# Kernel tuning notes

Measured on AMD Instinct MI355X. Metric: run time of the kernel, lower is better.

## Reference

```python
import jax, jax.numpy as jnp
import numpy as np

NEG_SLOPE = 0.2


def gat_conv(x, src, dst, W, a_src, a_dst, b, num_nodes):
    # x: [N, Fin], W: [Fin, Fout], a_src/a_dst: [Fout], b: [Fout]
    h = x @ W                                   # [N, Fout]
    alpha_s = h @ a_src                         # [N]
    alpha_d = h @ a_dst                         # [N]
    e = alpha_s[src] + alpha_d[dst]             # [E]
    e = jnp.where(e > 0, e, NEG_SLOPE * e)      # LeakyReLU(0.2)
    # segment softmax over edges grouped by destination node
    m = jax.ops.segment_max(e, dst, num_segments=num_nodes)   # [N]
    e = jnp.exp(e - m[dst])
    s = jax.ops.segment_sum(e, dst, num_segments=num_nodes)   # [N]
    alpha = e / s[dst]                          # [E] (every node has a self-loop)
    out = jax.ops.segment_sum(h[src] * alpha[:, None], dst, num_segments=num_nodes)
    return out + b


def setup_inputs() -> dict:
    key = jax.random.key(0)
    ks = jax.random.split(key, 10)
    N, E = 50000, 640000
    Fin, Fh, Fout = 128, 128, 64
    x = jax.random.normal(ks[0], (N, Fin), dtype=jnp.float32)
    edge_index = jax.random.randint(ks[1], (2, E), 0, N, dtype=jnp.int64)
    g = 1.0 / np.sqrt(Fin)
    W1 = jax.random.normal(ks[2], (Fin, Fh), dtype=jnp.float32) * g
    a1_src = jax.random.normal(ks[3], (Fh,), dtype=jnp.float32) * 0.1
    a1_dst = jax.random.normal(ks[4], (Fh,), dtype=jnp.float32) * 0.1
    b1 = jnp.zeros((Fh,), dtype=jnp.float32)
    g2 = 1.0 / np.sqrt(Fh)
    W2 = jax.random.normal(ks[5], (Fh, Fout), dtype=jnp.float32) * g2
    a2_src = jax.random.normal(ks[6], (Fout,), dtype=jnp.float32) * 0.1
    a2_dst = jax.random.normal(ks[7], (Fout,), dtype=jnp.float32) * 0.1
    b2 = jnp.zeros((Fout,), dtype=jnp.float32)
    return {"x": x, "edge_index": edge_index, "W1": W1, "a1_src": a1_src,
            "a1_dst": a1_dst, "b1": b1, "W2": W2, "a2_src": a2_src,
            "a2_dst": a2_dst, "b2": b2}


def reference(x, edge_index, W1, a1_src, a1_dst, b1, W2, a2_src, a2_dst, b2):
    N = x.shape[0]
    loops = jnp.arange(N, dtype=edge_index.dtype)
    src = jnp.concatenate([edge_index[0], loops])  # add self-loops (PyG default)
    dst = jnp.concatenate([edge_index[1], loops])
    h = gat_conv(x, src, dst, W1, a1_src, a1_dst, b1, N)
    h = jax.nn.relu(h)
    # F.dropout(0.1) skipped: deterministic (eval-mode) reference
    out = gat_conv(h, src, dst, W2, a2_src, a2_dst, b2, N)
    return out
```

## Files before the change

### kernel.cpp

```cpp
#include <hip/hip_runtime.h>

#define LEAK 0.2f

static __device__ __forceinline__ float leaky(float e) { return e > 0.f ? e : LEAK * e; }

static __device__ __forceinline__ unsigned f2bf(float f) {
    union { float f; unsigned u; } v; v.f = f;
    return (v.u + 0x7FFFu + ((v.u >> 16) & 1u)) >> 16;
}
static __device__ __forceinline__ float bflo(unsigned u) {
    union { unsigned x; float f; } v; v.x = u << 16; return v.f;
}
static __device__ __forceinline__ float bfhi(unsigned u) {
    union { unsigned x; float f; } v; v.x = u & 0xFFFF0000u; return v.f;
}

using bf16x8 = __attribute__((ext_vector_type(8))) short;
using f32x4 = __attribute__((ext_vector_type(4))) float;

__global__ __launch_bounds__(256) void k_prep(int* __restrict__ counts, int n,
                                              const int* __restrict__ ei, int nwords_check,
                                              int* __restrict__ flag,
                                              const float* __restrict__ W1,
                                              unsigned short* __restrict__ Wt1,
                                              const float* __restrict__ W2,
                                              unsigned short* __restrict__ Wt2, int NB) {
    int bid = blockIdx.x;
    int t = threadIdx.x;
    if (bid == 0) {
        if (t < 64) {
            int bad = 0;
            for (int i = 1 + 2 * t; i < nwords_check; i += 128) bad |= (ei[i] != 0);
            unsigned long long anybad = __ballot(bad != 0);
            if (t == 0) *flag = (anybad == 0ULL) ? 1 : 0;
        }
        return;
    }
    if (bid <= NB) {
        int i = (bid - 1) * 256 + t;
        if (i < n) counts[i] = 0;
        return;
    }
    if (bid <= NB + 4) {
        int q = bid - (NB + 1);
        int c = t & 127, ksub = t >> 7;
        int k0 = q * 32 + ksub * 16;
        union { unsigned short s[16]; uint4 v[2]; } u;
#pragma unroll
        for (int j = 0; j < 16; ++j) u.s[j] = (unsigned short)f2bf(W1[(size_t)(k0 + j) * 128 + c]);
        uint4* dst = (uint4*)(Wt1 + (size_t)c * 128 + k0);
        dst[0] = u.v[0];
        dst[1] = u.v[1];
        return;
    }
    {
        int q = bid - (NB + 5);
        int c = t & 63, ksub = t >> 6;
        int k0 = q * 64 + ksub * 16;
        union { unsigned short s[16]; uint4 v[2]; } u;
#pragma unroll
        for (int j = 0; j < 16; ++j) u.s[j] = (unsigned short)f2bf(W2[(size_t)(k0 + j) * 64 + c]);
        uint4* dst = (uint4*)(Wt2 + (size_t)c * 128 + k0);
        dst[0] = u.v[0];
        dst[1] = u.v[1];
        return;
    }
}

__global__ __launch_bounds__(256) void k_rank(const int* __restrict__ ei,
                                              const int* __restrict__ flag,
                                              int* __restrict__ counts,
                                              int* __restrict__ rank_,
                                              int* __restrict__ srcv,
                                              int* __restrict__ dstv, int E) {
    int base = (blockIdx.x * 256 + threadIdx.x) * 4;
    if (base >= E) return;
    int is64 = *flag;
    if (base + 3 < E) {
        int s0, s1, s2, s3, d0, d1, d2, d3;
        if (is64) {
            const uint4* ps = (const uint4*)(ei + 2 * (size_t)base);
            uint4 a = ps[0], b = ps[1];
            const uint4* pd = (const uint4*)(ei + 2 * ((size_t)E + base));
            uint4 c = pd[0], e4 = pd[1];
            s0 = a.x; s1 = a.z; s2 = b.x; s3 = b.z;
            d0 = c.x; d1 = c.z; d2 = e4.x; d3 = e4.z;
        } else {
            int4 a = *(const int4*)(ei + base);
            int4 b = *(const int4*)(ei + (size_t)E + base);
            s0 = a.x; s1 = a.y; s2 = a.z; s3 = a.w;
            d0 = b.x; d1 = b.y; d2 = b.z; d3 = b.w;
        }
        int r0 = atomicAdd(&counts[d0], 1);
        int r1 = atomicAdd(&counts[d1], 1);
        int r2 = atomicAdd(&counts[d2], 1);
        int r3 = atomicAdd(&counts[d3], 1);
        *(int4*)(rank_ + base) = make_int4(r0, r1, r2, r3);
        *(int4*)(srcv + base) = make_int4(s0, s1, s2, s3);
        *(int4*)(dstv + base) = make_int4(d0, d1, d2, d3);
    } else {
        for (int j = 0; j < 4 && base + j < E; ++j) {
            int e = base + j;
            int ss = is64 ? ei[2 * (size_t)e] : ei[e];
            int dd = is64 ? ei[2 * ((size_t)E + e)] : ei[(size_t)E + e];
            int r = atomicAdd(&counts[dd], 1);
            rank_[e] = r;
            srcv[e] = ss;
            dstv[e] = dd;
        }
    }
}

__global__ void k_scan1(const int* __restrict__ counts, int* __restrict__ incl,
                        int* __restrict__ bsums, int n) {
    __shared__ int s[256];
    int t = threadIdx.x;
    int g = blockIdx.x * 256 + t;
    int v = (g < n) ? counts[g] : 0;
    s[t] = v;
    __syncthreads();
    for (int off = 1; off < 256; off <<= 1) {
        int add = (t >= off) ? s[t - off] : 0;
        __syncthreads();
        s[t] += add;
        __syncthreads();
    }
    if (g < n) incl[g] = s[t];
    if (t == 255) bsums[blockIdx.x] = s[255];
}

__global__ void k_scan2(int* __restrict__ bsums, int nb) {
    __shared__ int s[256];
    int t = threadIdx.x;
    int v = (t < nb) ? bsums[t] : 0;
    s[t] = v;
    __syncthreads();
    for (int off = 1; off < 256; off <<= 1) {
        int add = (t >= off) ? s[t - off] : 0;
        __syncthreads();
        s[t] += add;
        __syncthreads();
    }
    int excl = (t == 0) ? 0 : s[t - 1];
    if (t < nb) bsums[t] = excl;
}

__global__ void k_scan3(const int* __restrict__ incl, const int* __restrict__ bsums,
                        int* __restrict__ rowptr, int n) {
    int g = blockIdx.x * 256 + threadIdx.x;
    if (g < n) rowptr[g + 1] = incl[g] + bsums[blockIdx.x];
    if (g == 0) rowptr[0] = 0;
}

__global__ __launch_bounds__(256) void k_place(const int* __restrict__ rank_,
                                               const int* __restrict__ srcv,
                                               const int* __restrict__ dstv,
                                               const int* __restrict__ rowptr,
                                               int* __restrict__ colv, int E) {
    int base = (blockIdx.x * 256 + threadIdx.x) * 4;
    if (base >= E) return;
    if (base + 3 < E) {
        int4 r = *(const int4*)(rank_ + base);
        int4 s = *(const int4*)(srcv + base);
        int4 d = *(const int4*)(dstv + base);
        int p0 = rowptr[d.x] + r.x;
        int p1 = rowptr[d.y] + r.y;
        int p2 = rowptr[d.z] + r.z;
        int p3 = rowptr[d.w] + r.w;
        colv[p0] = s.x;
        colv[p1] = s.y;
        colv[p2] = s.z;
        colv[p3] = s.w;
    } else {
        for (int j = 0; j < 4 && base + j < E; ++j) {
            int e = base + j;
            colv[rowptr[dstv[e]] + rank_[e]] = srcv[e];
        }
    }
}

template <int F, bool AF32>
__global__ __launch_bounds__(256) void k_gemm_mfma(const void* __restrict__ Xv,
                                                   const unsigned short* __restrict__ Wt,
                                                   const float* __restrict__ asrc,
                                                   const float* __restrict__ adst,
                                                   unsigned short* __restrict__ Hb,
                                                   float* __restrict__ out_s,
                                                   float* __restrict__ out_d, int n) {
    constexpr int K = 128;
    constexpr int KP = K + 8;
    constexpr int NT = F / 16;
    __shared__ unsigned short wsT[F * KP];
    int t = threadIdx.x;
    int w = t >> 6, lane = t & 63;
    int lrow = lane & 15, kg = lane >> 4;
    long long row0 = (long long)blockIdx.x * 64;

#pragma unroll
    for (int i = t; i < F * (K / 8); i += 256) {
        int c = i / (K / 8), j8 = i % (K / 8);
        uint4 v = ((const uint4*)(Wt + (size_t)c * K))[j8];
        *(uint4*)&wsT[c * KP + 8 * j8] = v;
    }
    __syncthreads();

    long long grow = row0 + w * 16 + lrow;
    bool rowok = grow < n;

    f32x4 acc[NT];
#pragma unroll
    for (int i = 0; i < NT; ++i) acc[i] = (f32x4){0.f, 0.f, 0.f, 0.f};

#pragma unroll
    for (int ks = 0; ks < K / 32; ++ks) {
        bf16x8 af;
        if constexpr (AF32) {
            const float* Xp = (const float*)Xv + grow * K + ks * 32 + kg * 8;
            float4 x0 = make_float4(0.f, 0.f, 0.f, 0.f), x1 = x0;
            if (rowok) {
                x0 = ((const float4*)Xp)[0];
                x1 = ((const float4*)Xp)[1];
            }
            af = (bf16x8){(short)f2bf(x0.x), (short)f2bf(x0.y), (short)f2bf(x0.z), (short)f2bf(x0.w),
                          (short)f2bf(x1.x), (short)f2bf(x1.y), (short)f2bf(x1.z), (short)f2bf(x1.w)};
        } else {
            uint4 u = make_uint4(0, 0, 0, 0);
            if (rowok) {
                const unsigned short* Xp = (const unsigned short*)Xv + grow * K + ks * 32 + kg * 8;
                u = *(const uint4*)Xp;
            }
            af = *(bf16x8*)&u;
        }
#pragma unroll
        for (int nt = 0; nt < NT; ++nt) {
            const unsigned short* bp = &wsT[(nt * 16 + lrow) * KP + ks * 32 + kg * 8];
            uint4 ub = *(const uint4*)bp;
            bf16x8 bf = *(bf16x8*)&ub;
            acc[nt] = __builtin_amdgcn_mfma_f32_16x16x32_bf16(af, bf, acc[nt], 0, 0, 0);
        }
    }

    {
        float ps[4] = {0.f, 0.f, 0.f, 0.f}, pd[4] = {0.f, 0.f, 0.f, 0.f};
#pragma unroll
        for (int nt = 0; nt < NT; ++nt) {
            float asv = asrc[nt * 16 + lrow];
            float adv = adst[nt * 16 + lrow];
#pragma unroll
            for (int i = 0; i < 4; ++i) {
                ps[i] = fmaf(acc[nt][i], asv, ps[i]);
                pd[i] = fmaf(acc[nt][i], adv, pd[i]);
            }
        }
#pragma unroll
        for (int off = 1; off < 16; off <<= 1) {
#pragma unroll
            for (int i = 0; i < 4; ++i) {
                ps[i] += __shfl_xor(ps[i], off);
                pd[i] += __shfl_xor(pd[i], off);
            }
        }
        if (lrow == 0) {
#pragma unroll
            for (int i = 0; i < 4; ++i) {
                long long r = row0 + w * 16 + kg * 4 + i;
                if (r < n) {
                    out_s[r] = ps[i];
                    out_d[r] = pd[i];
                }
            }
        }
    }

    int r0 = w * 16 + kg * 4;
#pragma unroll
    for (int nt = 0; nt < NT; ++nt) {
        int c = nt * 16 + lrow;
#pragma unroll
        for (int i = 0; i < 4; ++i) {
            long long r = row0 + r0 + i;
            if (r < n) Hb[r * F + c] = (unsigned short)f2bf(acc[nt][i]);
        }
    }
}

template <int F, bool RELU, bool OB>
__global__ __launch_bounds__(256) void k_agg(const int* __restrict__ rowptr,
                                             const int* __restrict__ colv,
                                             const float* __restrict__ as_,
                                             const float* __restrict__ ad_,
                                             const unsigned* __restrict__ Hu,
                                             const float* __restrict__ bias,
                                             void* __restrict__ OUT, int n) {
    constexpr int FG8 = F / 8;
    constexpr int GRP = 64 / FG8;
    int node = blockIdx.x * 4 + (threadIdx.x >> 6);
    int lane = threadIdx.x & 63;
    if (node >= n) return;
    int rs = rowptr[node], re = rowptr[node + 1];
    int deg = re - rs;
    float adi = ad_[node];
    float e_self = leaky(as_[node] + adi);

    int scol = node;
    float e_l = -3.0e38f;
    if (lane < deg) {
        scol = colv[rs + lane];
        e_l = leaky(as_[scol] + adi);
    }
    float m = fmaxf(e_l, e_self);
    for (int base = 64; base < deg; base += 64) {
        if (base + lane < deg) m = fmaxf(m, leaky(as_[colv[rs + base + lane]] + adi));
    }
#pragma unroll
    for (int off = 32; off; off >>= 1) m = fmaxf(m, __shfl_xor(m, off));

    float p_l = (lane < deg) ? __expf(e_l - m) : 0.f;
    float ssum = p_l;
    for (int base = 64; base < deg; base += 64) {
        if (base + lane < deg) ssum += __expf(leaky(as_[colv[rs + base + lane]] + adi) - m);
    }
#pragma unroll
    for (int off = 32; off; off >>= 1) ssum += __shfl_xor(ssum, off);
    float pself = __expf(e_self - m);
    ssum += pself;
    float inv = 1.f / ssum;
    float w_l = p_l * inv;
    float wself = pself * inv;

    int grp = lane / FG8;
    int fg = lane % FG8;
    const uint4* __restrict__ H16 = (const uint4*)Hu;
    float a0, a1, a2, a3, a4, a5, a6, a7;
    {
        uint4 hv = H16[(size_t)node * FG8 + fg];
        float ws0 = (grp == 0) ? wself : 0.f;
        a0 = ws0 * bflo(hv.x); a1 = ws0 * bfhi(hv.x);
        a2 = ws0 * bflo(hv.y); a3 = ws0 * bfhi(hv.y);
        a4 = ws0 * bflo(hv.z); a5 = ws0 * bfhi(hv.z);
        a6 = ws0 * bflo(hv.w); a7 = ws0 * bfhi(hv.w);
    }

    int cnt = deg < 64 ? deg : 64;
    constexpr int STEP = 4 * GRP;
    int cntr = (cnt + STEP - 1) / STEP * STEP;
#pragma unroll 1
    for (int i = 0; i < cntr; i += STEP) {
        int i0 = i + grp, i1 = i + GRP + grp, i2 = i + 2 * GRP + grp, i3 = i + 3 * GRP + grp;
        int s0 = __shfl(scol, i0), s1 = __shfl(scol, i1);
        int s2 = __shfl(scol, i2), s3 = __shfl(scol, i3);
        float w0 = __shfl(w_l, i0), w1 = __shfl(w_l, i1);
        float w2 = __shfl(w_l, i2), w3 = __shfl(w_l, i3);
        uint4 g0 = H16[(size_t)s0 * FG8 + fg];
        uint4 g1 = H16[(size_t)s1 * FG8 + fg];
        uint4 g2 = H16[(size_t)s2 * FG8 + fg];
        uint4 g3 = H16[(size_t)s3 * FG8 + fg];
        a0 = fmaf(w0, bflo(g0.x), a0); a1 = fmaf(w0, bfhi(g0.x), a1);
        a2 = fmaf(w0, bflo(g0.y), a2); a3 = fmaf(w0, bfhi(g0.y), a3);
        a4 = fmaf(w0, bflo(g0.z), a4); a5 = fmaf(w0, bfhi(g0.z), a5);
        a6 = fmaf(w0, bflo(g0.w), a6); a7 = fmaf(w0, bfhi(g0.w), a7);
        a0 = fmaf(w1, bflo(g1.x), a0); a1 = fmaf(w1, bfhi(g1.x), a1);
        a2 = fmaf(w1, bflo(g1.y), a2); a3 = fmaf(w1, bfhi(g1.y), a3);
        a4 = fmaf(w1, bflo(g1.z), a4); a5 = fmaf(w1, bfhi(g1.z), a5);
        a6 = fmaf(w1, bflo(g1.w), a6); a7 = fmaf(w1, bfhi(g1.w), a7);
        a0 = fmaf(w2, bflo(g2.x), a0); a1 = fmaf(w2, bfhi(g2.x), a1);
        a2 = fmaf(w2, bflo(g2.y), a2); a3 = fmaf(w2, bfhi(g2.y), a3);
        a4 = fmaf(w2, bflo(g2.z), a4); a5 = fmaf(w2, bfhi(g2.z), a5);
        a6 = fmaf(w2, bflo(g2.w), a6); a7 = fmaf(w2, bfhi(g2.w), a7);
        a0 = fmaf(w3, bflo(g3.x), a0); a1 = fmaf(w3, bfhi(g3.x), a1);
        a2 = fmaf(w3, bflo(g3.y), a2); a3 = fmaf(w3, bfhi(g3.y), a3);
        a4 = fmaf(w3, bflo(g3.z), a4); a5 = fmaf(w3, bfhi(g3.z), a5);
        a6 = fmaf(w3, bflo(g3.w), a6); a7 = fmaf(w3, bfhi(g3.w), a7);
    }
    for (int j = rs + 64; j < re; ++j) {
        int s = colv[j];
        float w = __expf(leaky(as_[s] + adi) - m) * inv;
        float we = (grp == 0) ? w : 0.f;
        uint4 g = H16[(size_t)s * FG8 + fg];
        a0 = fmaf(we, bflo(g.x), a0); a1 = fmaf(we, bfhi(g.x), a1);
        a2 = fmaf(we, bflo(g.y), a2); a3 = fmaf(we, bfhi(g.y), a3);
        a4 = fmaf(we, bflo(g.z), a4); a5 = fmaf(we, bfhi(g.z), a5);
        a6 = fmaf(we, bflo(g.w), a6); a7 = fmaf(we, bfhi(g.w), a7);
    }
#pragma unroll
    for (int off = FG8; off < 64; off <<= 1) {
        a0 += __shfl_xor(a0, off); a1 += __shfl_xor(a1, off);
        a2 += __shfl_xor(a2, off); a3 += __shfl_xor(a3, off);
        a4 += __shfl_xor(a4, off); a5 += __shfl_xor(a5, off);
        a6 += __shfl_xor(a6, off); a7 += __shfl_xor(a7, off);
    }
    if (grp == 0) {
        const float4* b4 = (const float4*)bias;
        float4 bv0 = b4[fg * 2], bv1 = b4[fg * 2 + 1];
        a0 += bv0.x; a1 += bv0.y; a2 += bv0.z; a3 += bv0.w;
        a4 += bv1.x; a5 += bv1.y; a6 += bv1.z; a7 += bv1.w;
        if (RELU) {
            a0 = fmaxf(a0, 0.f); a1 = fmaxf(a1, 0.f);
            a2 = fmaxf(a2, 0.f); a3 = fmaxf(a3, 0.f);
            a4 = fmaxf(a4, 0.f); a5 = fmaxf(a5, 0.f);
            a6 = fmaxf(a6, 0.f); a7 = fmaxf(a7, 0.f);
        }
        if (OB) {
            uint4 p;
            p.x = f2bf(a0) | (f2bf(a1) << 16);
            p.y = f2bf(a2) | (f2bf(a3) << 16);
            p.z = f2bf(a4) | (f2bf(a5) << 16);
            p.w = f2bf(a6) | (f2bf(a7) << 16);
            ((uint4*)OUT)[(size_t)node * FG8 + fg] = p;
        } else {
            float4* o4 = (float4*)((float*)OUT + (size_t)node * F + fg * 8);
            o4[0] = make_float4(a0, a1, a2, a3);
            o4[1] = make_float4(a4, a5, a6, a7);
        }
    }
}

extern "C" void kernel_launch(void* const* d_in, const int* in_sizes, int n_in,
                              void* d_out, int out_size, void* d_ws, size_t ws_size,
                              hipStream_t stream) {
    const float* x   = (const float*)d_in[0];
    const int*   ei  = (const int*)d_in[1];
    const float* W1  = (const float*)d_in[2];
    const float* a1s = (const float*)d_in[3];
    const float* a1d = (const float*)d_in[4];
    const float* b1  = (const float*)d_in[5];
    const float* W2  = (const float*)d_in[6];
    const float* a2s = (const float*)d_in[7];
    const float* a2d = (const float*)d_in[8];
    const float* b2  = (const float*)d_in[9];
    float* out = (float*)d_out;

    int N = in_sizes[0] / 128;
    int E = in_sizes[1] / 2;

    size_t off = 0;
    auto alloc = [&](size_t bytes) -> void* {
        off = (off + 255) & ~(size_t)255;
        void* p = (char*)d_ws + off;
        off += bytes;
        return p;
    };
    unsigned short* h = (unsigned short*)alloc((size_t)N * 128 * 2);
    unsigned short* out1b = (unsigned short*)alloc((size_t)N * 128 * 2);
    unsigned short* Wt1 = (unsigned short*)alloc(128 * 128 * 2);
    unsigned short* Wt2 = (unsigned short*)alloc(64 * 128 * 2);
    float* as_    = (float*)alloc((size_t)N * 4);
    float* ad_    = (float*)alloc((size_t)N * 4);
    int* counts   = (int*)alloc((size_t)N * 4);
    int* rowptr   = (int*)alloc((size_t)(N + 1) * 4);
    int* incl     = (int*)alloc((size_t)N * 4);
    int* bsums    = (int*)alloc(1024);
    int* colv     = (int*)alloc((size_t)E * 4);
    int* rank_    = (int*)alloc((size_t)E * 4);
    int* srcv     = (int*)alloc((size_t)E * 4);
    int* dstv     = (int*)alloc((size_t)E * 4);
    int* flag     = (int*)alloc(256);

    int NB = (N + 255) / 256;
    int blocksN4 = (N + 3) / 4;
    int rowTiles = (N + 63) / 64;
    int blocksE4 = (E + 1023) / 1024;

    int nchk = 2 * E < 512 ? 2 * E : 512;
    k_prep<<<NB + 7, 256, 0, stream>>>(counts, N, ei, nchk, flag, W1, Wt1, W2, Wt2, NB);
    k_rank<<<blocksE4, 256, 0, stream>>>(ei, flag, counts, rank_, srcv, dstv, E);
    k_scan1<<<NB, 256, 0, stream>>>(counts, incl, bsums, N);
    k_scan2<<<1, 256, 0, stream>>>(bsums, NB);
    k_scan3<<<NB, 256, 0, stream>>>(incl, bsums, rowptr, N);
    k_place<<<blocksE4, 256, 0, stream>>>(rank_, srcv, dstv, rowptr, colv, E);

    k_gemm_mfma<128, true><<<rowTiles, 256, 0, stream>>>(x, Wt1, a1s, a1d, h, as_, ad_, N);
    k_agg<128, true, true><<<blocksN4, 256, 0, stream>>>(rowptr, colv, as_, ad_,
                                                         (const unsigned*)h, b1, out1b, N);

    k_gemm_mfma<64, false><<<rowTiles, 256, 0, stream>>>(out1b, Wt2, a2s, a2d, h, as_, ad_, N);
    k_agg<64, false, false><<<blocksN4, 256, 0, stream>>>(rowptr, colv, as_, ad_,
                                                          (const unsigned*)h, b2, out, N);
}
```

Measured before the change: 139.7 us.

## Fuse CSR construction kernels into one cooperative kernel with grid syncs

Replaces the separate prep, rank, three-pass scan and place kernels with a single cooperative kernel. It uses grid-wide syncs between phases and runs a fixed grid of 256 blocks looping over the edges. Rank and destination are packed into one 32-bit word (rank in the high 16 bits, destination in the low 16), which removes the dstv and incl buffers and their memory traffic. The aim is to cut launch overhead and inter-kernel gaps. The trade-offs are grid.sync costs, less parallelism to hide atomic latency, and an implicit limit of N below 65536 and at most 256 scan chunks.

Result: slower. 250.1 us (+79.0%).

```diff
diff --git a/kernel.cpp b/kernel.cpp
--- a/kernel.cpp
+++ b/kernel.cpp
@@ -1,4 +1,7 @@
 #include <hip/hip_runtime.h>
+#include <hip/hip_cooperative_groups.h>
+
+namespace cg = cooperative_groups;
 
 #define LEAK 0.2f
 
@@ -18,163 +21,144 @@
 using bf16x8 = __attribute__((ext_vector_type(8))) short;
 using f32x4 = __attribute__((ext_vector_type(4))) float;
 
-__global__ __launch_bounds__(256) void k_prep(int* __restrict__ counts, int n,
-                                              const int* __restrict__ ei, int nwords_check,
-                                              int* __restrict__ flag,
-                                              const float* __restrict__ W1,
-                                              unsigned short* __restrict__ Wt1,
-                                              const float* __restrict__ W2,
-                                              unsigned short* __restrict__ Wt2, int NB) {
-    int bid = blockIdx.x;
-    int t = threadIdx.x;
+__global__ __launch_bounds__(256) void k_csr(const int* __restrict__ ei, int E, int N, int nchk,
+                                             int* __restrict__ flag, int* __restrict__ counts,
+                                             int* __restrict__ bsums, int* __restrict__ rowptr,
+                                             int* __restrict__ rankd, int* __restrict__ srcv,
+                                             int* __restrict__ colv,
+                                             const float* __restrict__ W1,
+                                             unsigned short* __restrict__ Wt1,
+                                             const float* __restrict__ W2,
+                                             unsigned short* __restrict__ Wt2) {
+    cg::grid_group grid = cg::this_grid();
+    __shared__ int s[256];
+    int t = threadIdx.x, bid = blockIdx.x;
+    int G = gridDim.x;
+    int gid = bid * 256 + t, GT = G * 256;
+
+    for (int i = gid; i < N; i += GT) counts[i] = 0;
     if (bid == 0) {
         if (t < 64) {
             int bad = 0;
-            for (int i = 1 + 2 * t; i < nwords_check; i += 128) bad |= (ei[i] != 0);
-            unsigned long long anybad = __ballot(bad != 0);
-            if (t == 0) *flag = (anybad == 0ULL) ? 1 : 0;
-        }
-        return;
-    }
-    if (bid <= NB) {
-        int i = (bid - 1) * 256 + t;
-        if (i < n) counts[i] = 0;
-        return;
-    }
-    if (bid <= NB + 4) {
-        int q = bid - (NB + 1);
+            for (int i = 1 + 2 * t; i < nchk; i += 128) bad |= (ei[i] != 0);
+            unsigned long long ab = __ballot(bad != 0);
+            if (t == 0) *flag = (ab == 0ULL) ? 1 : 0;
+        }
+    } else if (bid <= 4) {
+        int q = bid - 1;
         int c = t & 127, ksub = t >> 7;
         int k0 = q * 32 + ksub * 16;
-        union { unsigned short s[16]; uint4 v[2]; } u;
-#pragma unroll
-        for (int j = 0; j < 16; ++j) u.s[j] = (unsigned short)f2bf(W1[(size_t)(k0 + j) * 128 + c]);
+        union { unsigned short us[16]; uint4 v[2]; } u;
+#pragma unroll
+        for (int j = 0; j < 16; ++j) u.us[j] = (unsigned short)f2bf(W1[(size_t)(k0 + j) * 128 + c]);
         uint4* dst = (uint4*)(Wt1 + (size_t)c * 128 + k0);
         dst[0] = u.v[0];
         dst[1] = u.v[1];
-        return;
-    }
-    {
-        int q = bid - (NB + 5);
+    } else if (bid <= 6) {
+        int q = bid - 5;
         int c = t & 63, ksub = t >> 6;
         int k0 = q * 64 + ksub * 16;
-        union { unsigned short s[16]; uint4 v[2]; } u;
-#pragma unroll
-        for (int j = 0; j < 16; ++j) u.s[j] = (unsigned short)f2bf(W2[(size_t)(k0 + j) * 64 + c]);
+        union { unsigned short us[16]; uint4 v[2]; } u;
+#pragma unroll
+        for (int j = 0; j < 16; ++j) u.us[j] = (unsigned short)f2bf(W2[(size_t)(k0 + j) * 64 + c]);
         uint4* dst = (uint4*)(Wt2 + (size_t)c * 128 + k0);
         dst[0] = u.v[0];
         dst[1] = u.v[1];
-        return;
-    }
-}
-
-__global__ __launch_bounds__(256) void k_rank(const int* __restrict__ ei,
-                                              const int* __restrict__ flag,
-                                              int* __restrict__ counts,
-                                              int* __restrict__ rank_,
-                                              int* __restrict__ srcv,
-                                              int* __restrict__ dstv, int E) {
-    int base = (blockIdx.x * 256 + threadIdx.x) * 4;
-    if (base >= E) return;
-    int is64 = *flag;
-    if (base + 3 < E) {
-        int s0, s1, s2, s3, d0, d1, d2, d3;
-        if (is64) {
-            const uint4* ps = (const uint4*)(ei + 2 * (size_t)base);
-            uint4 a = ps[0], b = ps[1];
-            const uint4* pd = (const uint4*)(ei + 2 * ((size_t)E + base));
-            uint4 c = pd[0], e4 = pd[1];
-            s0 = a.x; s1 = a.z; s2 = b.x; s3 = b.z;
-            d0 = c.x; d1 = c.z; d2 = e4.x; d3 = e4.z;
+    }
+    grid.sync();
+
+    int is64 = *(volatile int*)flag;
+    for (long long base = (long long)gid * 4; base < E; base += (long long)GT * 4) {
+        if (base + 3 < E) {
+            int s0, s1, s2, s3, d0, d1, d2, d3;
+            if (is64) {
+                const uint4* ps = (const uint4*)(ei + 2 * base);
+                uint4 a = ps[0], b = ps[1];
+                const uint4* pd = (const uint4*)(ei + 2 * ((long long)E + base));
+                uint4 c4 = pd[0], e4 = pd[1];
+                s0 = a.x; s1 = a.z; s2 = b.x; s3 = b.z;
+                d0 = c4.x; d1 = c4.z; d2 = e4.x; d3 = e4.z;
+            } else {
+                int4 a = *(const int4*)(ei + base);
+                int4 b = *(const int4*)(ei + (long long)E + base);
+                s0 = a.x; s1 = a.y; s2 = a.z; s3 = a.w;
+                d0 = b.x; d1 = b.y; d2 = b.z; d3 = b.w;
+            }
+            int r0 = atomicAdd(&counts[d0], 1);
+            int r1 = atomicAdd(&counts[d1], 1);
+            int r2 = atomicAdd(&counts[d2], 1);
+            int r3 = atomicAdd(&counts[d3], 1);
+            *(int4*)(rankd + base) = make_int4((r0 << 16) | d0, (r1 << 16) | d1,
+                                               (r2 << 16) | d2, (r3 << 16) | d3);
+            *(int4*)(srcv + base) = make_int4(s0, s1, s2, s3);
         } else {
-            int4 a = *(const int4*)(ei + base);
-            int4 b = *(const int4*)(ei + (size_t)E + base);
-            s0 = a.x; s1 = a.y; s2 = a.z; s3 = a.w;
-            d0 = b.x; d1 = b.y; d2 = b.z; d3 = b.w;
-        }
-        int r0 = atomicAdd(&counts[d0], 1);
-        int r1 = atomicAdd(&counts[d1], 1);
-        int r2 = atomicAdd(&counts[d2], 1);
-        int r3 = atomicAdd(&counts[d3], 1);
-        *(int4*)(rank_ + base) = make_int4(r0, r1, r2, r3);
-        *(int4*)(srcv + base) = make_int4(s0, s1, s2, s3);
-        *(int4*)(dstv + base) = make_int4(d0, d1, d2, d3);
-    } else {
-        for (int j = 0; j < 4 && base + j < E; ++j) {
-            int e = base + j;
-            int ss = is64 ? ei[2 * (size_t)e] : ei[e];
-            int dd = is64 ? ei[2 * ((size_t)E + e)] : ei[(size_t)E + e];
-            int r = atomicAdd(&counts[dd], 1);
-            rank_[e] = r;
-            srcv[e] = ss;
-            dstv[e] = dd;
-        }
-    }
-}
-
-__global__ void k_scan1(const int* __restrict__ counts, int* __restrict__ incl,
-                        int* __restrict__ bsums, int n) {
-    __shared__ int s[256];
-    int t = threadIdx.x;
-    int g = blockIdx.x * 256 + t;
-    int v = (g < n) ? counts[g] : 0;
-    s[t] = v;
-    __syncthreads();
-    for (int off = 1; off < 256; off <<= 1) {
-        int add = (t >= off) ? s[t - off] : 0;
+            for (int j = 0; j < 4 && base + j < E; ++j) {
+                long long e = base + j;
+                int ss = is64 ? ei[2 * e] : ei[e];
+                int dd = is64 ? ei[2 * ((long long)E + e)] : ei[(long long)E + e];
+                int r = atomicAdd(&counts[dd], 1);
+                rankd[e] = (r << 16) | dd;
+                srcv[e] = ss;
+            }
+        }
+    }
+    grid.sync();
+
+    int NBc = (N + 255) / 256;
+    for (int c = bid; c < NBc; c += G) {
+        int g = c * 256 + t;
+        int v = (g < N) ? counts[g] : 0;
+        s[t] = v;
         __syncthreads();
-        s[t] += add;
+        for (int off = 1; off < 256; off <<= 1) {
+            int add = (t >= off) ? s[t - off] : 0;
+            __syncthreads();
+            s[t] += add;
+            __syncthreads();
+        }
+        if (g < N) rowptr[g + 1] = s[t];
+        if (t == 255) bsums[c] = s[255];
         __syncthreads();
     }
-    if (g < n) incl[g] = s[t];
-    if (t == 255) bsums[blockIdx.x] = s[255];
-}
-
-__global__ void k_scan2(int* __restrict__ bsums, int nb) {
-    __shared__ int s[256];
-    int t = threadIdx.x;
-    int v = (t < nb) ? bsums[t] : 0;
-    s[t] = v;
-    __syncthreads();
-    for (int off = 1; off < 256; off <<= 1) {
-        int add = (t >= off) ? s[t - off] : 0;
+    grid.sync();
+
+    {
+        int v = (t < NBc) ? bsums[t] : 0;
+        s[t] = v;
         __syncthreads();
-        s[t] += add;
-        __syncthreads();
-    }
-    int excl = (t == 0) ? 0 : s[t - 1];
-    if (t < nb) bsums[t] = excl;
-}
-
-__global__ void k_scan3(const int* __restrict__ incl, const int* __restrict__ bsums,
-                        int* __restrict__ rowptr, int n) {
-    int g = blockIdx.x * 256 + threadIdx.x;
-    if (g < n) rowptr[g + 1] = incl[g] + bsums[blockIdx.x];
-    if (g == 0) rowptr[0] = 0;
-}
-
-__global__ __launch_bounds__(256) void k_place(const int* __restrict__ rank_,
-                                               const int* __restrict__ srcv,
-                                               const int* __restrict__ dstv,
-                                               const int* __restrict__ rowptr,
-                                               int* __restrict__ colv, int E) {
-    int base = (blockIdx.x * 256 + threadIdx.x) * 4;
-    if (base >= E) return;
-    if (base + 3 < E) {
-        int4 r = *(const int4*)(rank_ + base);
-        int4 s = *(const int4*)(srcv + base);
-        int4 d = *(const int4*)(dstv + base);
-        int p0 = rowptr[d.x] + r.x;
-        int p1 = rowptr[d.y] + r.y;
-        int p2 = rowptr[d.z] + r.z;
-        int p3 = rowptr[d.w] + r.w;
-        colv[p0] = s.x;
-        colv[p1] = s.y;
-        colv[p2] = s.z;
-        colv[p3] = s.w;
-    } else {
-        for (int j = 0; j < 4 && base + j < E; ++j) {
-            int e = base + j;
-            colv[rowptr[dstv[e]] + rank_[e]] = srcv[e];
+        for (int off = 1; off < 256; off <<= 1) {
+            int add = (t >= off) ? s[t - off] : 0;
+            __syncthreads();
+            s[t] += add;
+            __syncthreads();
+        }
+        for (int c = bid; c < NBc; c += G) {
+            int pre = (c == 0) ? 0 : s[c - 1];
+            int g = c * 256 + t;
+            if (g < N) rowptr[g + 1] += pre;
+        }
+        if (gid == 0) rowptr[0] = 0;
+    }
+    grid.sync();
+
+    for (long long base = (long long)gid * 4; base < E; base += (long long)GT * 4) {
+        if (base + 3 < E) {
+            int4 rd = *(const int4*)(rankd + base);
+            int4 sv = *(const int4*)(srcv + base);
+            int p0 = rowptr[rd.x & 0xFFFF] + (rd.x >> 16);
+            int p1 = rowptr[rd.y & 0xFFFF] + (rd.y >> 16);
+            int p2 = rowptr[rd.z & 0xFFFF] + (rd.z >> 16);
+            int p3 = rowptr[rd.w & 0xFFFF] + (rd.w >> 16);
+            colv[p0] = sv.x;
+            colv[p1] = sv.y;
+            colv[p2] = sv.z;
+            colv[p3] = sv.w;
+        } else {
+            for (int j = 0; j < 4 && base + j < E; ++j) {
+                long long e = base + j;
+                int rd = rankd[e];
+                colv[rowptr[rd & 0xFFFF] + (rd >> 16)] = srcv[e];
+            }
         }
     }
 }
@@ -448,26 +432,23 @@
     float* ad_    = (float*)alloc((size_t)N * 4);
     int* counts   = (int*)alloc((size_t)N * 4);
     int* rowptr   = (int*)alloc((size_t)(N + 1) * 4);
-    int* incl     = (int*)alloc((size_t)N * 4);
     int* bsums    = (int*)alloc(1024);
     int* colv     = (int*)alloc((size_t)E * 4);
-    int* rank_    = (int*)alloc((size_t)E * 4);
+    int* rankd    = (int*)alloc((size_t)E * 4);
     int* srcv     = (int*)alloc((size_t)E * 4);
-    int* dstv     = (int*)alloc((size_t)E * 4);
     int* flag     = (int*)alloc(256);
 
-    int NB = (N + 255) / 256;
     int blocksN4 = (N + 3) / 4;
     int rowTiles = (N + 63) / 64;
-    int blocksE4 = (E + 1023) / 1024;
-
     int nchk = 2 * E < 512 ? 2 * E : 512;
-    k_prep<<<NB + 7, 256, 0, stream>>>(counts, N, ei, nchk, flag, W1, Wt1, W2, Wt2, NB);
-    k_rank<<<blocksE4, 256, 0, stream>>>(ei, flag, counts, rank_, srcv, dstv, E);
-    k_scan1<<<NB, 256, 0, stream>>>(counts, incl, bsums, N);
-    k_scan2<<<1, 256, 0, stream>>>(bsums, NB);
-    k_scan3<<<NB, 256, 0, stream>>>(incl, bsums, rowptr, N);
-    k_place<<<blocksE4, 256, 0, stream>>>(rank_, srcv, dstv, rowptr, colv, E);
+
+    {
+        void* args[] = {(void*)&ei, (void*)&E, (void*)&N, (void*)&nchk,
+                        (void*)&flag, (void*)&counts, (void*)&bsums, (void*)&rowptr,
+                        (void*)&rankd, (void*)&srcv, (void*)&colv,
+                        (void*)&W1, (void*)&Wt1, (void*)&W2, (void*)&Wt2};
+        hipLaunchCooperativeKernel((void*)k_csr, dim3(256), dim3(256), args, 0, stream);
+    }
 
     k_gemm_mfma<128, true><<<rowTiles, 256, 0, stream>>>(x, Wt1, a1s, a1d, h, as_, ad_, N);
     k_agg<128, true, true><<<blocksN4, 256, 0, stream>>>(rowptr, colv, as_, ad_,
```

## Fuse CSR placement into first GEMM launch and pack rank with destination

Applied to the files above, without the earlier changes.

The separate k_place kernel is removed. Its scatter work now runs in extra blocks appended to the first MFMA GEMM grid, so CSR column placement overlaps with the layer-1 projection and one launch disappears. k_rank now packs each edge's per-node rank and destination id into one 32-bit word (rank in the high 16 bits, dst in the low 16 bits). This drops the separate dstv and rank arrays and their traffic. The packing is only correct when the node count and per-node in-degree fit in 16 bits, which the current sizes satisfy but general inputs may not.

New measurement: 135.4 us. -3.0%, faster.

```diff
diff --git a/kernel.cpp b/kernel.cpp
--- a/kernel.cpp
+++ b/kernel.cpp
@@ -70,9 +70,8 @@
 __global__ __launch_bounds__(256) void k_rank(const int* __restrict__ ei,
                                               const int* __restrict__ flag,
                                               int* __restrict__ counts,
-                                              int* __restrict__ rank_,
-                                              int* __restrict__ srcv,
-                                              int* __restrict__ dstv, int E) {
+                                              int* __restrict__ rankd,
+                                              int* __restrict__ srcv, int E) {
     int base = (blockIdx.x * 256 + threadIdx.x) * 4;
     if (base >= E) return;
     int is64 = *flag;
@@ -95,18 +94,17 @@
         int r1 = atomicAdd(&counts[d1], 1);
         int r2 = atomicAdd(&counts[d2], 1);
         int r3 = atomicAdd(&counts[d3], 1);
-        *(int4*)(rank_ + base) = make_int4(r0, r1, r2, r3);
+        *(int4*)(rankd + base) = make_int4((r0 << 16) | d0, (r1 << 16) | d1,
+                                           (r2 << 16) | d2, (r3 << 16) | d3);
         *(int4*)(srcv + base) = make_int4(s0, s1, s2, s3);
-        *(int4*)(dstv + base) = make_int4(d0, d1, d2, d3);
     } else {
         for (int j = 0; j < 4 && base + j < E; ++j) {
             int e = base + j;
             int ss = is64 ? ei[2 * (size_t)e] : ei[e];
             int dd = is64 ? ei[2 * ((size_t)E + e)] : ei[(size_t)E + e];
             int r = atomicAdd(&counts[dd], 1);
-            rank_[e] = r;
+            rankd[e] = (r << 16) | dd;
             srcv[e] = ss;
-            dstv[e] = dd;
         }
     }
 }
@@ -152,33 +150,6 @@
     if (g == 0) rowptr[0] = 0;
 }
 
-__global__ __launch_bounds__(256) void k_place(const int* __restrict__ rank_,
-                                               const int* __restrict__ srcv,
-                                               const int* __restrict__ dstv,
-                                               const int* __restrict__ rowptr,
-                                               int* __restrict__ colv, int E) {
-    int base = (blockIdx.x * 256 + threadIdx.x) * 4;
-    if (base >= E) return;
-    if (base + 3 < E) {
-        int4 r = *(const int4*)(rank_ + base);
-        int4 s = *(const int4*)(srcv + base);
-        int4 d = *(const int4*)(dstv + base);
-        int p0 = rowptr[d.x] + r.x;
-        int p1 = rowptr[d.y] + r.y;
-        int p2 = rowptr[d.z] + r.z;
-        int p3 = rowptr[d.w] + r.w;
-        colv[p0] = s.x;
-        colv[p1] = s.y;
-        colv[p2] = s.z;
-        colv[p3] = s.w;
-    } else {
-        for (int j = 0; j < 4 && base + j < E; ++j) {
-            int e = base + j;
-            colv[rowptr[dstv[e]] + rank_[e]] = srcv[e];
-        }
-    }
-}
-
 template <int F, bool AF32>
 __global__ __launch_bounds__(256) void k_gemm_mfma(const void* __restrict__ Xv,
                                                    const unsigned short* __restrict__ Wt,
@@ -186,12 +157,42 @@
                                                    const float* __restrict__ adst,
                                                    unsigned short* __restrict__ Hb,
                                                    float* __restrict__ out_s,
-                                                   float* __restrict__ out_d, int n) {
+                                                   float* __restrict__ out_d, int n,
+                                                   int rowTiles,
+                                                   const int* __restrict__ rankd,
+                                                   const int* __restrict__ srcv,
+                                                   const int* __restrict__ rowptr,
+                                                   int* __restrict__ colv, int E) {
     constexpr int K = 128;
     constexpr int KP = K + 8;
     constexpr int NT = F / 16;
     __shared__ unsigned short wsT[F * KP];
     int t = threadIdx.x;
+
+    if (blockIdx.x >= rowTiles) {
+        int base = ((blockIdx.x - rowTiles) * 256 + t) * 4;
+        if (base >= E) return;
+        if (base + 3 < E) {
+            int4 rd = *(const int4*)(rankd + base);
+            int4 sv = *(const int4*)(srcv + base);
+            int p0 = rowptr[rd.x & 0xFFFF] + (rd.x >> 16);
+            int p1 = rowptr[rd.y & 0xFFFF] + (rd.y >> 16);
+            int p2 = rowptr[rd.z & 0xFFFF] + (rd.z >> 16);
+            int p3 = rowptr[rd.w & 0xFFFF] + (rd.w >> 16);
+            colv[p0] = sv.x;
+            colv[p1] = sv.y;
+            colv[p2] = sv.z;
+            colv[p3] = sv.w;
+        } else {
+            for (int j = 0; j < 4 && base + j < E; ++j) {
+                int e = base + j;
+                int rd = rankd[e];
+                colv[rowptr[rd & 0xFFFF] + (rd >> 16)] = srcv[e];
+            }
+        }
+        return;
+    }
+
     int w = t >> 6, lane = t & 63;
     int lrow = lane & 15, kg = lane >> 4;
     long long row0 = (long long)blockIdx.x * 64;
@@ -451,9 +452,8 @@
     int* incl     = (int*)alloc((size_t)N * 4);
     int* bsums    = (int*)alloc(1024);
     int* colv     = (int*)alloc((size_t)E * 4);
-    int* rank_    = (int*)alloc((size_t)E * 4);
+    int* rankd    = (int*)alloc((size_t)E * 4);
     int* srcv     = (int*)alloc((size_t)E * 4);
-    int* dstv     = (int*)alloc((size_t)E * 4);
     int* flag     = (int*)alloc(256);
 
     int NB = (N + 255) / 256;
@@ -463,17 +463,18 @@
 
     int nchk = 2 * E < 512 ? 2 * E : 512;
     k_prep<<<NB + 7, 256, 0, stream>>>(counts, N, ei, nchk, flag, W1, Wt1, W2, Wt2, NB);
-    k_rank<<<blocksE4, 256, 0, stream>>>(ei, flag, counts, rank_, srcv, dstv, E);
+    k_rank<<<blocksE4, 256, 0, stream>>>(ei, flag, counts, rankd, srcv, E);
     k_scan1<<<NB, 256, 0, stream>>>(counts, incl, bsums, N);
     k_scan2<<<1, 256, 0, stream>>>(bsums, NB);
     k_scan3<<<NB, 256, 0, stream>>>(incl, bsums, rowptr, N);
-    k_place<<<blocksE4, 256, 0, stream>>>(rank_, srcv, dstv, rowptr, colv, E);
-
-    k_gemm_mfma<128, true><<<rowTiles, 256, 0, stream>>>(x, Wt1, a1s, a1d, h, as_, ad_, N);
+
+    k_gemm_mfma<128, true><<<rowTiles + blocksE4, 256, 0, stream>>>(
+        x, Wt1, a1s, a1d, h, as_, ad_, N, rowTiles, rankd, srcv, rowptr, colv, E);
     k_agg<128, true, true><<<blocksN4, 256, 0, stream>>>(rowptr, colv, as_, ad_,
                                                          (const unsigned*)h, b1, out1b, N);
 
-    k_gemm_mfma<64, false><<<rowTiles, 256, 0, stream>>>(out1b, Wt2, a2s, a2d, h, as_, ad_, N);
+    k_gemm_mfma<64, false><<<rowTiles, 256, 0, stream>>>(
+        out1b, Wt2, a2s, a2d, h, as_, ad_, N, rowTiles, rankd, srcv, rowptr, colv, 0);
     k_agg<64, false, false><<<blocksN4, 256, 0, stream>>>(rowptr, colv, as_, ad_,
                                                           (const unsigned*)h, b2, out, N);
 }
```
